# Performance work log

Measured on AMD Instinct MI355X. Metric: run time of the kernel, lower is better.

Reference implementation:

```python
import jax, jax.numpy as jnp
import numpy as np

B, N, IN_CH = 16, 2048, 128
H, C = 4, 64
HC = H * C
E = 524288
NT = B * N
FC0, FC1 = 1024, 512
OMIC = 128
OUT = 2
LN_EPS = 1e-5


def setup_inputs() -> dict:
    key = jax.random.key(0)
    ks = jax.random.split(key, 32)
    s = 0.02
    d = {}
    d['x'] = jax.random.normal(ks[0], (NT, IN_CH), jnp.float32)
    d['edge_index'] = jax.random.randint(ks[1], (2, E), 0, NT, dtype=jnp.int64)
    # GATConv 1: Linear(IN_CH, H*C, bias=False), att_src/att_dst [H,C], bias [H*C]
    d['w1'] = jax.random.normal(ks[2], (IN_CH, HC), jnp.float32) * s
    d['att_src1'] = jax.random.normal(ks[3], (H, C), jnp.float32) * s
    d['att_dst1'] = jax.random.normal(ks[4], (H, C), jnp.float32) * s
    d['bias1'] = jnp.zeros((HC,), jnp.float32)
    d['pool1_w'] = jax.random.normal(ks[5], (HC, 1), jnp.float32) * s
    d['pool1_b'] = jnp.zeros((1,), jnp.float32)
    # GATConv 2: in = H*C
    d['w2'] = jax.random.normal(ks[6], (HC, HC), jnp.float32) * s
    d['att_src2'] = jax.random.normal(ks[7], (H, C), jnp.float32) * s
    d['att_dst2'] = jax.random.normal(ks[8], (H, C), jnp.float32) * s
    d['bias2'] = jnp.zeros((HC,), jnp.float32)
    d['pool2_w'] = jax.random.normal(ks[9], (HC, 1), jnp.float32) * s
    d['pool2_b'] = jnp.zeros((1,), jnp.float32)
    # LayerNorm(num_nodes)
    d['ln_w'] = jnp.ones((N,), jnp.float32)
    d['ln_b'] = jnp.zeros((N,), jnp.float32)
    # FC encoder: Linear(3N, FC0)+ELU, Linear(FC0, FC1)+ELU, Linear(FC1, OMIC)+ELU
    d['enc0_w'] = jax.random.normal(ks[10], (3 * N, FC0), jnp.float32) * s
    d['enc0_b'] = jnp.zeros((FC0,), jnp.float32)
    d['enc1_w'] = jax.random.normal(ks[11], (FC0, FC1), jnp.float32) * s
    d['enc1_b'] = jnp.zeros((FC1,), jnp.float32)
    d['enc2_w'] = jax.random.normal(ks[12], (FC1, OMIC), jnp.float32) * s
    d['enc2_b'] = jnp.zeros((OMIC,), jnp.float32)
    d['last_w'] = jax.random.normal(ks[13], (OMIC, OUT), jnp.float32) * s
    d['last_b'] = jnp.zeros((OUT,), jnp.float32)
    return d


def layer_norm(v, w, b):
    mu = jnp.mean(v, axis=-1, keepdims=True)
    var = jnp.mean((v - mu) ** 2, axis=-1, keepdims=True)
    return (v - mu) * jax.lax.rsqrt(var + LN_EPS) * w + b


def gat_conv(x, src, dst, w, att_src, att_dst, bias):
    # x: [NT, F_in] -> transformed per head [NT, H, C]
    xw = (x @ w).reshape(NT, H, C)
    a_src = jnp.einsum('nhc,hc->nh', xw, att_src)  # [NT, H]
    a_dst = jnp.einsum('nhc,hc->nh', xw, att_dst)
    alpha = jax.nn.leaky_relu(a_src[src] + a_dst[dst], negative_slope=0.2)  # [E', H]
    amax = jax.ops.segment_max(alpha, dst, num_segments=NT)
    ea = jnp.exp(alpha - amax[dst])
    denom = jax.ops.segment_sum(ea, dst, num_segments=NT)
    coef = ea / (denom[dst] + 1e-16)
    msg = xw[src] * coef[:, :, None]  # [E', H, C]
    out = jax.ops.segment_sum(msg, dst, num_segments=NT)
    return out.reshape(NT, HC) + bias


def reference(x, edge_index, w1, att_src1, att_dst1, bias1, pool1_w, pool1_b,
              w2, att_src2, att_dst2, bias2, pool2_w, pool2_b,
              ln_w, ln_b, enc0_w, enc0_b, enc1_w, enc1_b, enc2_w, enc2_b,
              last_w, last_b):
    # add self-loops (GATConv default)
    loops = jnp.arange(NT, dtype=edge_index.dtype)
    src = jnp.concatenate([edge_index[0], loops])
    dst = jnp.concatenate([edge_index[1], loops])
    # layer1 feature: per-node mean, densified to [B, N]
    x0 = layer_norm(jnp.mean(x, axis=-1).reshape(B, N), ln_w, ln_b)
    # GAT layer 1 (dropout is identity in eval)
    h = jax.nn.elu(gat_conv(x, src, dst, w1, att_src1, att_dst1, bias1))
    x1 = layer_norm((h @ pool1_w + pool1_b)[:, 0].reshape(B, N), ln_w, ln_b)
    # GAT layer 2
    h = jax.nn.elu(gat_conv(h, src, dst, w2, att_src2, att_dst2, bias2))
    x2 = layer_norm((h @ pool2_w + pool2_b)[:, 0].reshape(B, N), ln_w, ln_b)
    feat = jnp.concatenate([x0, x1, x2], axis=1)  # [B, 3N]
    e = jax.nn.elu(feat @ enc0_w + enc0_b)
    e = jax.nn.elu(e @ enc1_w + enc1_b)
    e = jax.nn.elu(e @ enc2_w + enc2_b)
    return e @ last_w + last_b  # [B, OUT]
```

## Files before the change

### kernel.cpp

```cpp
#include <hip/hip_runtime.h>
#include <math.h>

#define NTN 32768
#define BB 16
#define NN 2048
#define IN_CH 128
#define HC 256
#define EREAL 524288
#define ETOT (EREAL + NTN)
#define FC0 1024
#define FC1 512
#define OMIC 128
#define OUTD 2
#define CAP 96

#define PREP_BLKS (NTN / 4)
#define DEG_BLKS (EREAL / 256)
#define CASTW_BLKS ((HC * IN_CH + HC * HC) / 256)
#define GEMM_YB (NTN / 128)
#define FILL_YB 512

typedef __attribute__((ext_vector_type(8))) short bf16x8;
typedef __attribute__((ext_vector_type(4))) float f32x4;
typedef __attribute__((ext_vector_type(2))) float f32x2;

static __device__ __forceinline__ float wave_sum(float v) {
    for (int o = 32; o; o >>= 1) v += __shfl_xor(v, o);
    return v;
}
static __device__ __forceinline__ unsigned short f2bf(float f) {
    unsigned u = __float_as_uint(f);
    unsigned r = (u + 0x7fff + ((u >> 16) & 1)) >> 16;
    return (unsigned short)r;
}
static __device__ __forceinline__ void wave_sync() {
    asm volatile("s_waitcnt lgkmcnt(0)" ::: "memory");
    __builtin_amdgcn_sched_barrier(0);
}
static __device__ __forceinline__ void pkfma(f32x2& acc, f32x2 ab, f32x2 e2) {
    asm("v_pk_fma_f32 %0, %1, %2, %0" : "+v"(acc) : "v"(ab), "v"(e2));
}
static __device__ __forceinline__ void fma8pk(uint4 v, f32x2 e2, f32x2* acc) {
    f32x2 p;
    p.x = __uint_as_float(v.x << 16); p.y = __uint_as_float(v.x & 0xffff0000u);
    pkfma(acc[0], p, e2);
    p.x = __uint_as_float(v.y << 16); p.y = __uint_as_float(v.y & 0xffff0000u);
    pkfma(acc[1], p, e2);
    p.x = __uint_as_float(v.z << 16); p.y = __uint_as_float(v.z & 0xffff0000u);
    pkfma(acc[2], p, e2);
    p.x = __uint_as_float(v.w << 16); p.y = __uint_as_float(v.w & 0xffff0000u);
    pkfma(acc[3], p, e2);
}
static __device__ __forceinline__ void dot2bf(float& acc, unsigned px, unsigned pe) {
    asm("v_dot2_f32_bf16 %0, %1, %2, %0" : "+v"(acc) : "v"(px), "v"(pe));
}
static __device__ __forceinline__ void dot8x2(uint4 a, uint4 b, unsigned pe, float* acc) {
    unsigned p;
    p = __builtin_amdgcn_perm(a.x, b.x, 0x01000504u); dot2bf(acc[0], p, pe);
    p = __builtin_amdgcn_perm(a.x, b.x, 0x03020706u); dot2bf(acc[1], p, pe);
    p = __builtin_amdgcn_perm(a.y, b.y, 0x01000504u); dot2bf(acc[2], p, pe);
    p = __builtin_amdgcn_perm(a.y, b.y, 0x03020706u); dot2bf(acc[3], p, pe);
    p = __builtin_amdgcn_perm(a.z, b.z, 0x01000504u); dot2bf(acc[4], p, pe);
    p = __builtin_amdgcn_perm(a.z, b.z, 0x03020706u); dot2bf(acc[5], p, pe);
    p = __builtin_amdgcn_perm(a.w, b.w, 0x01000504u); dot2bf(acc[6], p, pe);
    p = __builtin_amdgcn_perm(a.w, b.w, 0x03020706u); dot2bf(acc[7], p, pe);
}

__global__ __launch_bounds__(256) void k_pre(
    const float* __restrict__ x, unsigned short* __restrict__ xb, float* __restrict__ xmean,
    const int* __restrict__ ei, int* __restrict__ deg, int* __restrict__ epos,
    const float* __restrict__ w1, const float* __restrict__ w2,
    unsigned short* __restrict__ w1t, unsigned short* __restrict__ w2t) {
    int b = blockIdx.x, t = threadIdx.x;
    if (b < PREP_BLKS) {
        int wave = t >> 6, lane = t & 63;
        int n = b * 4 + wave;
        float2 v = *(const float2*)(x + (size_t)n * IN_CH + lane * 2);
        ushort2 o;
        o.x = f2bf(v.x); o.y = f2bf(v.y);
        *(ushort2*)(xb + (size_t)n * IN_CH + lane * 2) = o;
        float s = wave_sum(v.x + v.y);
        if (lane == 0) xmean[n] = s * (1.0f / 128.0f);
    } else if (b < PREP_BLKS + DEG_BLKS) {
        int e = (b - PREP_BLKS) * 256 + t;
        int d = ei[EREAL + e];
        epos[e] = atomicAdd(&deg[d], 1);
    } else {
        int idx = (b - PREP_BLKS - DEG_BLKS) * 256 + t;
        if (idx < HC * IN_CH) {
            int n = idx / IN_CH, k = idx % IN_CH;
            w1t[idx] = f2bf(w1[(size_t)k * HC + n]);
        } else {
            int j = idx - HC * IN_CH;
            int n = j / HC, k = j % HC;
            w2t[j] = f2bf(w2[(size_t)k * HC + n]);
        }
    }
}

__global__ __launch_bounds__(1024) void k_scan(const int* __restrict__ deg, int* __restrict__ rowptr,
                                               int* __restrict__ csr) {
    __shared__ int sd[1024];
    int t = threadIdx.x;
    int base = t * 32;
    int loc[32];
    int s = 0;
#pragma unroll
    for (int j = 0; j < 32; j++) { int d = deg[base + j] + 1; loc[j] = d; s += d; }
    sd[t] = s; __syncthreads();
    for (int o = 1; o < 1024; o <<= 1) {
        int v = (t >= o) ? sd[t - o] : 0;
        __syncthreads();
        sd[t] += v;
        __syncthreads();
    }
    int run = sd[t] - s;
#pragma unroll
    for (int j = 0; j < 32; j++) {
        rowptr[base + j] = run;
        csr[run] = base + j;
        run += loc[j];
    }
    if (t == 1023) rowptr[NTN] = run;
}

__global__ __launch_bounds__(256) void k_gemm_mfma(
    const unsigned short* __restrict__ A, const unsigned short* __restrict__ Bt, int K,
    const float* __restrict__ attS, const float* __restrict__ attD,
    unsigned short* __restrict__ Cout, float* __restrict__ aS, float* __restrict__ aD,
    const int* __restrict__ ei, const int* __restrict__ epos,
    const int* __restrict__ rowptr, int* __restrict__ csr) {
    __shared__ unsigned short As[128][72];
    __shared__ unsigned short Bs[64][72];
    const int t = threadIdx.x;
    const int bx = blockIdx.x, by = blockIdx.y;
    if (by >= GEMM_YB) {
        int e = (((by - GEMM_YB) * 4 + bx)) * 256 + t;
        int s = ei[e], d = ei[EREAL + e];
        csr[rowptr[d] + 1 + epos[e]] = s;
        return;
    }
    const int lane = t & 63, wave = t >> 6;
    const int quad = lane >> 4, l16 = lane & 15;
    const int arow = t >> 1, acol = (t & 1) * 32;
    const int brow = t >> 2, bcol = (t & 3) * 16;
    const unsigned short* Ag = A + (size_t)(by * 128 + arow) * K + acol;
    const unsigned short* Bg = Bt + (size_t)(bx * 64 + brow) * K + bcol;
    f32x4 acc[2][4] = {};
    for (int k0 = 0; k0 < K; k0 += 64) {
        uint4 a0 = *(const uint4*)(Ag + k0);
        uint4 a1 = *(const uint4*)(Ag + k0 + 8);
        uint4 a2 = *(const uint4*)(Ag + k0 + 16);
        uint4 a3 = *(const uint4*)(Ag + k0 + 24);
        uint4 b0 = *(const uint4*)(Bg + k0);
        uint4 b1 = *(const uint4*)(Bg + k0 + 8);
        __syncthreads();
        *(uint4*)&As[arow][acol +  0] = a0;
        *(uint4*)&As[arow][acol +  8] = a1;
        *(uint4*)&As[arow][acol + 16] = a2;
        *(uint4*)&As[arow][acol + 24] = a3;
        *(uint4*)&Bs[brow][bcol +  0] = b0;
        *(uint4*)&Bs[brow][bcol +  8] = b1;
        __syncthreads();
#pragma unroll
        for (int kc = 0; kc < 64; kc += 32) {
            bf16x8 af[2], bfr[4];
#pragma unroll
            for (int mt = 0; mt < 2; mt++)
                af[mt] = *(const bf16x8*)&As[wave * 32 + mt * 16 + l16][kc + quad * 8];
#pragma unroll
            for (int nt = 0; nt < 4; nt++)
                bfr[nt] = *(const bf16x8*)&Bs[nt * 16 + l16][kc + quad * 8];
#pragma unroll
            for (int mt = 0; mt < 2; mt++)
#pragma unroll
                for (int nt = 0; nt < 4; nt++)
                    acc[mt][nt] = __builtin_amdgcn_mfma_f32_16x16x32_bf16(af[mt], bfr[nt], acc[mt][nt], 0, 0, 0);
        }
    }
    float as_l[4], ad_l[4];
#pragma unroll
    for (int nt = 0; nt < 4; nt++) {
        int gcol = bx * 64 + nt * 16 + l16;
        as_l[nt] = attS[gcol];
        ad_l[nt] = attD[gcol];
    }
#pragma unroll
    for (int mt = 0; mt < 2; mt++) {
#pragma unroll
        for (int reg = 0; reg < 4; reg++) {
            int grow = by * 128 + wave * 32 + mt * 16 + quad * 4 + reg;
            float ps = 0.f, pd = 0.f;
#pragma unroll
            for (int nt = 0; nt < 4; nt++) {
                float v = acc[mt][nt][reg];
                Cout[(size_t)grow * HC + bx * 64 + nt * 16 + l16] = f2bf(v);
                ps += v * as_l[nt];
                pd += v * ad_l[nt];
            }
            for (int o = 8; o; o >>= 1) { ps += __shfl_xor(ps, o); pd += __shfl_xor(pd, o); }
            if (l16 == 0) { aS[grow * 4 + bx] = ps; aD[grow * 4 + bx] = pd; }
        }
    }
}

__global__ __launch_bounds__(256) void k_agg(
    const unsigned short* __restrict__ xw, const float* __restrict__ aS, const float* __restrict__ aD,
    const int* __restrict__ rowptr, const int* __restrict__ csr,
    const float* __restrict__ bias, const float* __restrict__ poolw, const float* __restrict__ poolb,
    unsigned short* __restrict__ hout, float* __restrict__ xpre) {
    __shared__ float ea_s[4][CAP][4];
    __shared__ int   ss[4][CAP];
    int t = threadIdx.x;
    int w = t >> 6, lane = t & 63;
    int n = blockIdx.x * 4 + w;
    int beg = rowptr[n], end = rowptr[n + 1];
    int deg = end - beg;
    float4 ad4 = *(const float4*)(aD + n * 4);
    float l0 = 0.f, l1 = 0.f, l2 = 0.f, l3 = 0.f;
    if (deg <= CAP) {
        for (int i = lane; i < deg; i += 64) {
            int s = csr[beg + i];
            ss[w][i] = s << 9;
            float4 as4 = *(const float4*)(aS + s * 4);
            float a0 = as4.x + ad4.x; a0 = a0 > 0.f ? a0 : 0.2f * a0;
            float a1 = as4.y + ad4.y; a1 = a1 > 0.f ? a1 : 0.2f * a1;
            float a2 = as4.z + ad4.z; a2 = a2 > 0.f ? a2 : 0.2f * a2;
            float a3 = as4.w + ad4.w; a3 = a3 > 0.f ? a3 : 0.2f * a3;
            float4 e4;
            e4.x = __expf(a0); e4.y = __expf(a1); e4.z = __expf(a2); e4.w = __expf(a3);
            *(float4*)&ea_s[w][i][0] = e4;
        }
        wave_sync();
    } else {
        for (int i = lane; i < deg; i += 64) {
            int s = csr[beg + i];
            float4 as4 = *(const float4*)(aS + s * 4);
            float a0 = as4.x + ad4.x; a0 = a0 > 0.f ? a0 : 0.2f * a0; l0 += __expf(a0);
            float a1 = as4.y + ad4.y; a1 = a1 > 0.f ? a1 : 0.2f * a1; l1 += __expf(a1);
            float a2 = as4.z + ad4.z; a2 = a2 > 0.f ? a2 : 0.2f * a2; l2 += __expf(a2);
            float a3 = as4.w + ad4.w; a3 = a3 > 0.f ? a3 : 0.2f * a3; l3 += __expf(a3);
        }
        l0 = wave_sum(l0); l1 = wave_sum(l1); l2 = wave_sum(l2); l3 = wave_sum(l3);
    }
    int l31 = lane & 31, hi = lane >> 5;
    int head = l31 >> 3;
    float acc8[8] = {};
    f32x2 accF[4] = {};
    unsigned tb = (unsigned)(l31 * 16);
    const char* xwb_ = (const char*)xw;
    if (deg <= CAP) {
        int i = 0;
        for (; i + 16 <= deg; i += 16) {
            int iA = i + 8 * hi;
            int o0 = ss[w][iA], o1 = ss[w][iA + 1], o2 = ss[w][iA + 2], o3 = ss[w][iA + 3];
            int o4 = ss[w][iA + 4], o5 = ss[w][iA + 5], o6 = ss[w][iA + 6], o7 = ss[w][iA + 7];
            float e0 = ea_s[w][iA][head],     e1 = ea_s[w][iA + 1][head];
            float e2 = ea_s[w][iA + 2][head], e3 = ea_s[w][iA + 3][head];
            float e4 = ea_s[w][iA + 4][head], e5 = ea_s[w][iA + 5][head];
            float e6 = ea_s[w][iA + 6][head], e7 = ea_s[w][iA + 7][head];
            uint4 v0 = *(const uint4*)(xwb_ + ((unsigned)o0 + tb));
            uint4 v1 = *(const uint4*)(xwb_ + ((unsigned)o1 + tb));
            uint4 v2 = *(const uint4*)(xwb_ + ((unsigned)o2 + tb));
            uint4 v3 = *(const uint4*)(xwb_ + ((unsigned)o3 + tb));
            uint4 v4 = *(const uint4*)(xwb_ + ((unsigned)o4 + tb));
            uint4 v5 = *(const uint4*)(xwb_ + ((unsigned)o5 + tb));
            uint4 v6 = *(const uint4*)(xwb_ + ((unsigned)o6 + tb));
            uint4 v7 = *(const uint4*)(xwb_ + ((unsigned)o7 + tb));
            unsigned p01, p23, p45, p67;
            asm("v_cvt_pk_bf16_f32 %0, %1, %2" : "=v"(p01) : "v"(e0), "v"(e1));
            asm("v_cvt_pk_bf16_f32 %0, %1, %2" : "=v"(p23) : "v"(e2), "v"(e3));
            asm("v_cvt_pk_bf16_f32 %0, %1, %2" : "=v"(p45) : "v"(e4), "v"(e5));
            asm("v_cvt_pk_bf16_f32 %0, %1, %2" : "=v"(p67) : "v"(e6), "v"(e7));
            dot8x2(v0, v1, p01, acc8);
            dot8x2(v2, v3, p23, acc8);
            dot8x2(v4, v5, p45, acc8);
            dot8x2(v6, v7, p67, acc8);
        }
        for (; i + 8 <= deg; i += 8) {
            int iA = i + 4 * hi;
            int o0 = ss[w][iA], o1 = ss[w][iA + 1], o2 = ss[w][iA + 2], o3 = ss[w][iA + 3];
            float e0 = ea_s[w][iA][head],     e1 = ea_s[w][iA + 1][head];
            float e2 = ea_s[w][iA + 2][head], e3 = ea_s[w][iA + 3][head];
            uint4 v0 = *(const uint4*)(xwb_ + ((unsigned)o0 + tb));
            uint4 v1 = *(const uint4*)(xwb_ + ((unsigned)o1 + tb));
            uint4 v2 = *(const uint4*)(xwb_ + ((unsigned)o2 + tb));
            uint4 v3 = *(const uint4*)(xwb_ + ((unsigned)o3 + tb));
            unsigned p01, p23;
            asm("v_cvt_pk_bf16_f32 %0, %1, %2" : "=v"(p01) : "v"(e0), "v"(e1));
            asm("v_cvt_pk_bf16_f32 %0, %1, %2" : "=v"(p23) : "v"(e2), "v"(e3));
            dot8x2(v0, v1, p01, acc8);
            dot8x2(v2, v3, p23, acc8);
        }
        for (; i + 4 <= deg; i += 4) {
            int iA = i + 2 * hi;
            int o0 = ss[w][iA], o1 = ss[w][iA + 1];
            float e0 = ea_s[w][iA][head], e1 = ea_s[w][iA + 1][head];
            unsigned pe;
            asm("v_cvt_pk_bf16_f32 %0, %1, %2" : "=v"(pe) : "v"(e0), "v"(e1));
            uint4 v0 = *(const uint4*)(xwb_ + ((unsigned)o0 + tb));
            uint4 v1 = *(const uint4*)(xwb_ + ((unsigned)o1 + tb));
            dot8x2(v0, v1, pe, acc8);
        }
        if (i < deg) {
            int iA = i + 2 * hi, iB = iA + 1;
            bool okA = iA < deg, okB = iB < deg;
            int ia = okA ? iA : 0;
            int ib = okB ? iB : 0;
            int o0 = ss[w][ia], o1 = ss[w][ib];
            float e0 = okA ? ea_s[w][ia][head] : 0.f;
            float e1 = okB ? ea_s[w][ib][head] : 0.f;
            unsigned pe;
            asm("v_cvt_pk_bf16_f32 %0, %1, %2" : "=v"(pe) : "v"(e0), "v"(e1));
            uint4 v0 = *(const uint4*)(xwb_ + ((unsigned)o0 + tb));
            uint4 v1 = *(const uint4*)(xwb_ + ((unsigned)o1 + tb));
            dot8x2(v0, v1, pe, acc8);
        }
    } else {
        const unsigned short* xwc = xw + l31 * 8;
        float adh = head == 0 ? ad4.x : head == 1 ? ad4.y : head == 2 ? ad4.z : ad4.w;
        for (int i = beg; i < end; i += 2) {
            int idx = i + hi;
            bool ok = idx < end;
            int sA = csr[ok ? idx : beg];
            float a = aS[sA * 4 + head] + adh;
            a = a > 0.f ? a : 0.2f * a;
            float eA = ok ? __expf(a) : 0.f;
            uint4 vA = *(const uint4*)(xwc + (size_t)sA * HC);
            f32x2 eA2; eA2.x = eA; eA2.y = eA;
            fma8pk(vA, eA2, accF);
        }
    }
    float r8[8];
#pragma unroll
    for (int j = 0; j < 8; j++) {
        float v = acc8[j] + accF[j >> 1][j & 1];
        v += __shfl_xor(v, 32);
        r8[j] = v;
    }
    if (hi == 0) {
        float ilh;
        if (deg <= CAP) {
            float lsum = 0.f;
            for (int j = (l31 & 7); j < deg; j += 8) lsum += ea_s[w][j][head];
            lsum += __shfl_xor(lsum, 1);
            lsum += __shfl_xor(lsum, 2);
            lsum += __shfl_xor(lsum, 4);
            ilh = 1.0f / (lsum + 1e-16f);
        } else {
            float lh = head == 0 ? l0 : head == 1 ? l1 : head == 2 ? l2 : l3;
            ilh = 1.0f / (lh + 1e-16f);
        }
        float4 b0 = *(const float4*)(bias + l31 * 8);
        float4 b1 = *(const float4*)(bias + l31 * 8 + 4);
        float r[8];
        r[0] = r8[0] * ilh + b0.x;
        r[1] = r8[1] * ilh + b0.y;
        r[2] = r8[2] * ilh + b0.z;
        r[3] = r8[3] * ilh + b0.w;
        r[4] = r8[4] * ilh + b1.x;
        r[5] = r8[5] * ilh + b1.y;
        r[6] = r8[6] * ilh + b1.z;
        r[7] = r8[7] * ilh + b1.w;
#pragma unroll
        for (int j = 0; j < 8; j++) r[j] = r[j] > 0.f ? r[j] : expm1f(r[j]);
        if (hout) {
            uint4 o;
            o.x = (unsigned)f2bf(r[0]) | ((unsigned)f2bf(r[1]) << 16);
            o.y = (unsigned)f2bf(r[2]) | ((unsigned)f2bf(r[3]) << 16);
            o.z = (unsigned)f2bf(r[4]) | ((unsigned)f2bf(r[5]) << 16);
            o.w = (unsigned)f2bf(r[6]) | ((unsigned)f2bf(r[7]) << 16);
            *(uint4*)(hout + (size_t)n * HC + l31 * 8) = o;
        }
        float4 w0 = *(const float4*)(poolw + l31 * 8);
        float4 w1v = *(const float4*)(poolw + l31 * 8 + 4);
        float p = r[0] * w0.x + r[1] * w0.y + r[2] * w0.z + r[3] * w0.w +
                  r[4] * w1v.x + r[5] * w1v.y + r[6] * w1v.z + r[7] * w1v.w;
        for (int o = 16; o; o >>= 1) p += __shfl_xor(p, o);
        if (l31 == 0) xpre[n] = p + poolb[0];
    }
}

__global__ __launch_bounds__(256) void k_ln3(const float* __restrict__ xmean, const float* __restrict__ x1pre,
                                             const float* __restrict__ x2pre, const float* __restrict__ lw,
                                             const float* __restrict__ lb, float* __restrict__ feat) {
    __shared__ float r0[256], r1[256];
    int b = blockIdx.x, t = threadIdx.x;
    int row = b & 15, seg = b >> 4;
    const float* src = (seg == 0 ? xmean : seg == 1 ? x1pre : x2pre) + (size_t)row * NN;
    float* dst = feat + (size_t)row * (3 * NN) + seg * NN;
    float v[8];
    float s = 0.f, s2 = 0.f;
#pragma unroll
    for (int j = 0; j < 8; j++) {
        float x = src[t + j * 256];
        v[j] = x; s += x; s2 += x * x;
    }
    r0[t] = s; r1[t] = s2; __syncthreads();
    for (int o = 128; o; o >>= 1) {
        if (t < o) { r0[t] += r0[t + o]; r1[t] += r1[t + o]; }
        __syncthreads();
    }
    float mu = r0[0] * (1.0f / NN);
    float var = r1[0] * (1.0f / NN) - mu * mu;
    float rs = rsqrtf(var + 1e-5f);
#pragma unroll
    for (int j = 0; j < 8; j++) {
        int idx = t + j * 256;
        dst[idx] = (v[j] - mu) * rs * lw[idx] + lb[idx];
    }
}

template<int KC>
__global__ __launch_bounds__(256) void k_fc_splitk(const float* __restrict__ In, const float* __restrict__ W,
                                                   float* __restrict__ partial, int K, int Nc) {
    __shared__ float in_s[16][KC];
    int t = threadIdx.x;
    int k0 = blockIdx.y * KC;
    for (int idx = t; idx < 16 * KC; idx += 256) {
        int r = idx / KC, kk = idx % KC;
        in_s[r][kk] = In[(size_t)r * K + k0 + kk];
    }
    __syncthreads();
    int col = blockIdx.x * 256 + t;
    if (col < Nc) {
        float acc[16] = {};
#pragma unroll
        for (int kk = 0; kk < KC; kk++) {
            float w = W[(size_t)(k0 + kk) * Nc + col];
#pragma unroll
            for (int r = 0; r < 16; r++) acc[r] += in_s[r][kk] * w;
        }
        float* pp = partial + ((size_t)blockIdx.y * 16) * Nc + col;
#pragma unroll
        for (int r = 0; r < 16; r++) pp[(size_t)r * Nc] = acc[r];
    }
}

template<int KS>
__global__ __launch_bounds__(256) void k_fc_reduce(const float* __restrict__ partial, const float* __restrict__ bias,
                                                   float* __restrict__ Out, int Nc) {
    __shared__ float sm[256];
    int t = threadIdx.x;
    int col = blockIdx.x * 32 + (t & 31);
    int r = blockIdx.y;
    int h = t >> 5;
    float s = 0.f;
#pragma unroll
    for (int i = 0; i < KS / 8; i++)
        s += partial[((size_t)(h + 8 * i) * 16 + r) * Nc + col];
    sm[t] = s;
    __syncthreads();
    if (t < 32) {
        float v = sm[t] + sm[t + 32] + sm[t + 64] + sm[t + 96] +
                  sm[t + 128] + sm[t + 160] + sm[t + 192] + sm[t + 224];
        v += bias[col];
        v = v > 0.f ? v : expm1f(v);
        Out[(size_t)r * Nc + col] = v;
    }
}

__global__ __launch_bounds__(256) void k_last(const float* __restrict__ In, const float* __restrict__ W,
                                              const float* __restrict__ b, float* __restrict__ Out) {
    int t = threadIdx.x;
    int r = t >> 4, c = (t >> 3) & 1, ksub = t & 7;
    float s = 0.f;
#pragma unroll
    for (int k = 0; k < OMIC / 8; k++) s += In[r * OMIC + k * 8 + ksub] * W[(k * 8 + ksub) * OUTD + c];
    for (int o = 1; o < 8; o <<= 1) s += __shfl_xor(s, o);
    if (ksub == 0) Out[r * OUTD + c] = s + b[c];
}

extern "C" void kernel_launch(void* const* d_in, const int* in_sizes, int n_in,
                              void* d_out, int out_size, void* d_ws, size_t ws_size,
                              hipStream_t stream) {
    (void)in_sizes; (void)n_in; (void)out_size; (void)ws_size;
    const float* x        = (const float*)d_in[0];
    const int*   ei       = (const int*)d_in[1];
    const float* w1       = (const float*)d_in[2];
    const float* att_src1 = (const float*)d_in[3];
    const float* att_dst1 = (const float*)d_in[4];
    const float* bias1    = (const float*)d_in[5];
    const float* pool1_w  = (const float*)d_in[6];
    const float* pool1_b  = (const float*)d_in[7];
    const float* w2       = (const float*)d_in[8];
    const float* att_src2 = (const float*)d_in[9];
    const float* att_dst2 = (const float*)d_in[10];
    const float* bias2    = (const float*)d_in[11];
    const float* pool2_w  = (const float*)d_in[12];
    const float* pool2_b  = (const float*)d_in[13];
    const float* ln_w     = (const float*)d_in[14];
    const float* ln_b     = (const float*)d_in[15];
    const float* enc0_w   = (const float*)d_in[16];
    const float* enc0_b   = (const float*)d_in[17];
    const float* enc1_w   = (const float*)d_in[18];
    const float* enc1_b   = (const float*)d_in[19];
    const float* enc2_w   = (const float*)d_in[20];
    const float* enc2_b   = (const float*)d_in[21];
    const float* last_w   = (const float*)d_in[22];
    const float* last_b   = (const float*)d_in[23];
    float* out = (float*)d_out;

    char* p = (char*)d_ws;
    auto alloc = [&](size_t bytes) -> void* {
        void* r = (void*)p;
        p += (bytes + 255) & ~(size_t)255;
        return r;
    };
    unsigned short* xwb  = (unsigned short*)alloc((size_t)NTN * HC * 2);
    unsigned short* hb   = (unsigned short*)alloc((size_t)NTN * HC * 2);
    unsigned short* xb   = (unsigned short*)alloc((size_t)NTN * IN_CH * 2);
    unsigned short* w1t  = (unsigned short*)alloc((size_t)HC * IN_CH * 2);
    unsigned short* w2t  = (unsigned short*)alloc((size_t)HC * HC * 2);
    float* a_src  = (float*)alloc((size_t)NTN * 4 * 4);
    float* a_dst  = (float*)alloc((size_t)NTN * 4 * 4);
    float* xmean  = (float*)alloc((size_t)NTN * 4);
    float* x1pre  = (float*)alloc((size_t)NTN * 4);
    float* x2pre  = (float*)alloc((size_t)NTN * 4);
    float* feat   = (float*)alloc((size_t)BB * 3 * NN * 4);
    float* e0     = (float*)alloc((size_t)BB * FC0 * 4);
    float* e1     = (float*)alloc((size_t)BB * FC1 * 4);
    float* e2     = (float*)alloc((size_t)BB * OMIC * 4);
    float* part0  = (float*)alloc((size_t)96 * 16 * FC0 * 4);
    float* part1  = (float*)alloc((size_t)64 * 16 * FC1 * 4);
    float* part2  = (float*)alloc((size_t)32 * 16 * OMIC * 4);
    int*   deg    = (int*)alloc((size_t)NTN * 4);
    int*   rowptr = (int*)alloc((size_t)(NTN + 1) * 4);
    int*   epos   = (int*)alloc((size_t)EREAL * 4);
    int*   csr    = (int*)alloc((size_t)ETOT * 4);

    hipMemsetAsync(deg, 0, (size_t)NTN * 4, stream);

    k_pre<<<PREP_BLKS + DEG_BLKS + CASTW_BLKS, 256, 0, stream>>>(
        x, xb, xmean, ei, deg, epos, w1, w2, w1t, w2t);
    k_scan<<<1, 1024, 0, stream>>>(deg, rowptr, csr);

    k_gemm_mfma<<<dim3(4, GEMM_YB + FILL_YB), 256, 0, stream>>>(
        xb, w1t, IN_CH, att_src1, att_dst1, xwb, a_src, a_dst, ei, epos, rowptr, csr);
    k_agg<<<NTN / 4, 256, 0, stream>>>(xwb, a_src, a_dst, rowptr, csr, bias1, pool1_w, pool1_b, hb, x1pre);

    k_gemm_mfma<<<dim3(4, GEMM_YB), 256, 0, stream>>>(
        hb, w2t, HC, att_src2, att_dst2, xwb, a_src, a_dst, ei, epos, rowptr, csr);
    k_agg<<<NTN / 4, 256, 0, stream>>>(xwb, a_src, a_dst, rowptr, csr, bias2, pool2_w, pool2_b, (unsigned short*)nullptr, x2pre);

    k_ln3<<<48, 256, 0, stream>>>(xmean, x1pre, x2pre, ln_w, ln_b, feat);

    k_fc_splitk<64><<<dim3(4, 96), 256, 0, stream>>>(feat, enc0_w, part0, 3 * NN, FC0);
    k_fc_reduce<96><<<dim3(FC0 / 32, 16), 256, 0, stream>>>(part0, enc0_b, e0, FC0);
    k_fc_splitk<16><<<dim3(2, 64), 256, 0, stream>>>(e0, enc1_w, part1, FC0, FC1);
    k_fc_reduce<64><<<dim3(FC1 / 32, 16), 256, 0, stream>>>(part1, enc1_b, e1, FC1);
    k_fc_splitk<16><<<dim3(1, 32), 256, 0, stream>>>(e1, enc2_w, part2, FC1, OMIC);
    k_fc_reduce<32><<<dim3(OMIC / 32, 16), 256, 0, stream>>>(part2, enc2_b, e2, OMIC);
    k_last<<<1, 256, 0, stream>>>(e2, last_w, last_b, out);
}
```

Before: 315.7 us.

## Fuse LayerNorm and FC encoder head into one cooperative kernel with grid syncs

Replaces the eight small launches (LayerNorm, three split-K FC layers with their reductions, and the final linear) with a single cooperative kernel of 384 blocks that separates the stages with grid-wide syncs. The aim is to remove per-launch overhead and inter-kernel gaps in the tail of the pipeline. In exchange it adds grid-barrier cost, leaves many blocks idle in the later stages, and makes the split-K inner loop non-templated, with a runtime KC and no unrolling.

Result: slower. 660.7 us (+109.3%).

```diff
diff --git a/kernel.cpp b/kernel.cpp
--- a/kernel.cpp
+++ b/kernel.cpp
@@ -1,5 +1,8 @@
 #include <hip/hip_runtime.h>
+#include <hip/hip_cooperative_groups.h>
 #include <math.h>
+
+namespace cg = cooperative_groups;
 
 #define NTN 32768
 #define BB 16
@@ -381,94 +384,108 @@
     }
 }
 
-__global__ __launch_bounds__(256) void k_ln3(const float* __restrict__ xmean, const float* __restrict__ x1pre,
-                                             const float* __restrict__ x2pre, const float* __restrict__ lw,
-                                             const float* __restrict__ lb, float* __restrict__ feat) {
-    __shared__ float r0[256], r1[256];
-    int b = blockIdx.x, t = threadIdx.x;
-    int row = b & 15, seg = b >> 4;
-    const float* src = (seg == 0 ? xmean : seg == 1 ? x1pre : x2pre) + (size_t)row * NN;
-    float* dst = feat + (size_t)row * (3 * NN) + seg * NN;
-    float v[8];
-    float s = 0.f, s2 = 0.f;
-#pragma unroll
-    for (int j = 0; j < 8; j++) {
-        float x = src[t + j * 256];
-        v[j] = x; s += x; s2 += x * x;
-    }
-    r0[t] = s; r1[t] = s2; __syncthreads();
-    for (int o = 128; o; o >>= 1) {
-        if (t < o) { r0[t] += r0[t + o]; r1[t] += r1[t + o]; }
-        __syncthreads();
-    }
-    float mu = r0[0] * (1.0f / NN);
-    float var = r1[0] * (1.0f / NN) - mu * mu;
-    float rs = rsqrtf(var + 1e-5f);
-#pragma unroll
-    for (int j = 0; j < 8; j++) {
-        int idx = t + j * 256;
-        dst[idx] = (v[j] - mu) * rs * lw[idx] + lb[idx];
-    }
-}
-
-template<int KC>
-__global__ __launch_bounds__(256) void k_fc_splitk(const float* __restrict__ In, const float* __restrict__ W,
-                                                   float* __restrict__ partial, int K, int Nc) {
-    __shared__ float in_s[16][KC];
-    int t = threadIdx.x;
-    int k0 = blockIdx.y * KC;
+
+static __device__ __forceinline__ void splitk_body(
+    const float* __restrict__ In, const float* __restrict__ W, float* __restrict__ partial,
+    int K, int Nc, int KC, int bx, int by, int t, float* in_s ) {
+    int k0 = by * KC;
     for (int idx = t; idx < 16 * KC; idx += 256) {
         int r = idx / KC, kk = idx % KC;
-        in_s[r][kk] = In[(size_t)r * K + k0 + kk];
+        in_s[r * KC + kk] = In[(size_t)r * K + k0 + kk];
     }
     __syncthreads();
-    int col = blockIdx.x * 256 + t;
+    int col = bx * 256 + t;
     if (col < Nc) {
         float acc[16] = {};
-#pragma unroll
         for (int kk = 0; kk < KC; kk++) {
             float w = W[(size_t)(k0 + kk) * Nc + col];
 #pragma unroll
-            for (int r = 0; r < 16; r++) acc[r] += in_s[r][kk] * w;
-        }
-        float* pp = partial + ((size_t)blockIdx.y * 16) * Nc + col;
+            for (int r = 0; r < 16; r++) acc[r] += in_s[r * KC + kk] * w;
+        }
+        float* pp = partial + ((size_t)by * 16) * Nc + col;
 #pragma unroll
         for (int r = 0; r < 16; r++) pp[(size_t)r * Nc] = acc[r];
     }
 }
 
 template<int KS>
-__global__ __launch_bounds__(256) void k_fc_reduce(const float* __restrict__ partial, const float* __restrict__ bias,
-                                                   float* __restrict__ Out, int Nc) {
-    __shared__ float sm[256];
-    int t = threadIdx.x;
-    int col = blockIdx.x * 32 + (t & 31);
-    int r = blockIdx.y;
-    int h = t >> 5;
-    float s = 0.f;
-#pragma unroll
-    for (int i = 0; i < KS / 8; i++)
-        s += partial[((size_t)(h + 8 * i) * 16 + r) * Nc + col];
-    sm[t] = s;
-    __syncthreads();
-    if (t < 32) {
-        float v = sm[t] + sm[t + 32] + sm[t + 64] + sm[t + 96] +
-                  sm[t + 128] + sm[t + 160] + sm[t + 192] + sm[t + 224];
-        v += bias[col];
-        v = v > 0.f ? v : expm1f(v);
-        Out[(size_t)r * Nc + col] = v;
-    }
-}
-
-__global__ __launch_bounds__(256) void k_last(const float* __restrict__ In, const float* __restrict__ W,
-                                              const float* __restrict__ b, float* __restrict__ Out) {
-    int t = threadIdx.x;
-    int r = t >> 4, c = (t >> 3) & 1, ksub = t & 7;
-    float s = 0.f;
-#pragma unroll
-    for (int k = 0; k < OMIC / 8; k++) s += In[r * OMIC + k * 8 + ksub] * W[(k * 8 + ksub) * OUTD + c];
-    for (int o = 1; o < 8; o <<= 1) s += __shfl_xor(s, o);
-    if (ksub == 0) Out[r * OUTD + c] = s + b[c];
+static __device__ __forceinline__ void reduce_body(
+    const float* __restrict__ partial, const float* __restrict__ bias, float* __restrict__ Out,
+    int Nc, int b, int t, int nb) {
+    for (int idx = b * 256 + t; idx < 16 * Nc; idx += nb * 256) {
+        int r = idx / Nc, col = idx - r * Nc;
+        float s = 0.f;
+#pragma unroll 8
+        for (int k = 0; k < KS; k++) s += partial[((size_t)k * 16 + r) * Nc + col];
+        s += bias[col];
+        Out[(size_t)r * Nc + col] = s > 0.f ? s : expm1f(s);
+    }
+}
+
+#define HEAD_BLKS 384
+
+__global__ __launch_bounds__(256) void k_head(
+    const float* __restrict__ xmean, const float* __restrict__ x1pre, const float* __restrict__ x2pre,
+    const float* __restrict__ lw, const float* __restrict__ lb, float* __restrict__ feat,
+    const float* __restrict__ enc0_w, const float* __restrict__ enc0_b,
+    const float* __restrict__ enc1_w, const float* __restrict__ enc1_b,
+    const float* __restrict__ enc2_w, const float* __restrict__ enc2_b,
+    const float* __restrict__ last_w, const float* __restrict__ last_b,
+    float* __restrict__ e0, float* __restrict__ e1, float* __restrict__ e2,
+    float* __restrict__ part0, float* __restrict__ part1, float* __restrict__ part2,
+    float* __restrict__ out) {
+    cg::grid_group gg = cg::this_grid();
+    __shared__ float lds[16 * 64];
+    int b = blockIdx.x, t = threadIdx.x;
+
+    if (b < 48) {
+        float* r0 = lds;
+        float* r1 = lds + 256;
+        int row = b & 15, seg = b >> 4;
+        const float* src = (seg == 0 ? xmean : seg == 1 ? x1pre : x2pre) + (size_t)row * NN;
+        float* dst = feat + (size_t)row * (3 * NN) + seg * NN;
+        float v[8];
+        float s = 0.f, s2 = 0.f;
+#pragma unroll
+        for (int j = 0; j < 8; j++) {
+            float x = src[t + j * 256];
+            v[j] = x; s += x; s2 += x * x;
+        }
+        r0[t] = s; r1[t] = s2; __syncthreads();
+        for (int o = 128; o; o >>= 1) {
+            if (t < o) { r0[t] += r0[t + o]; r1[t] += r1[t + o]; }
+            __syncthreads();
+        }
+        float mu = r0[0] * (1.0f / NN);
+        float var = r1[0] * (1.0f / NN) - mu * mu;
+        float rs = rsqrtf(var + 1e-5f);
+#pragma unroll
+        for (int j = 0; j < 8; j++) {
+            int idx = t + j * 256;
+            dst[idx] = (v[j] - mu) * rs * lw[idx] + lb[idx];
+        }
+    }
+    gg.sync();
+    splitk_body(feat, enc0_w, part0, 3 * NN, FC0, 64, b & 3, b >> 2, t, lds);
+    gg.sync();
+    reduce_body<96>(part0, enc0_b, e0, FC0, b, t, HEAD_BLKS);
+    gg.sync();
+    if (b < 128) splitk_body(e0, enc1_w, part1, FC0, FC1, 16, b & 1, b >> 1, t, lds);
+    gg.sync();
+    reduce_body<64>(part1, enc1_b, e1, FC1, b, t, HEAD_BLKS);
+    gg.sync();
+    if (b < 32) splitk_body(e1, enc2_w, part2, FC1, OMIC, 16, 0, b, t, lds);
+    gg.sync();
+    reduce_body<32>(part2, enc2_b, e2, OMIC, b, t, HEAD_BLKS);
+    gg.sync();
+    if (b == 0) {
+        int r = t >> 4, c = (t >> 3) & 1, ksub = t & 7;
+        float s = 0.f;
+#pragma unroll
+        for (int k = 0; k < OMIC / 8; k++) s += e2[r * OMIC + k * 8 + ksub] * last_w[(k * 8 + ksub) * OUTD + c];
+        for (int o = 1; o < 8; o <<= 1) s += __shfl_xor(s, o);
+        if (ksub == 0) out[r * OUTD + c] = s + last_b[c];
+    }
 }
 
 extern "C" void kernel_launch(void* const* d_in, const int* in_sizes, int n_in,
@@ -543,13 +560,15 @@
         hb, w2t, HC, att_src2, att_dst2, xwb, a_src, a_dst, ei, epos, rowptr, csr);
     k_agg<<<NTN / 4, 256, 0, stream>>>(xwb, a_src, a_dst, rowptr, csr, bias2, pool2_w, pool2_b, (unsigned short*)nullptr, x2pre);
 
-    k_ln3<<<48, 256, 0, stream>>>(xmean, x1pre, x2pre, ln_w, ln_b, feat);
-
-    k_fc_splitk<64><<<dim3(4, 96), 256, 0, stream>>>(feat, enc0_w, part0, 3 * NN, FC0);
-    k_fc_reduce<96><<<dim3(FC0 / 32, 16), 256, 0, stream>>>(part0, enc0_b, e0, FC0);
-    k_fc_splitk<16><<<dim3(2, 64), 256, 0, stream>>>(e0, enc1_w, part1, FC0, FC1);
-    k_fc_reduce<64><<<dim3(FC1 / 32, 16), 256, 0, stream>>>(part1, enc1_b, e1, FC1);
-    k_fc_splitk<16><<<dim3(1, 32), 256, 0, stream>>>(e1, enc2_w, part2, FC1, OMIC);
-    k_fc_reduce<32><<<dim3(OMIC / 32, 16), 256, 0, stream>>>(part2, enc2_b, e2, OMIC);
-    k_last<<<1, 256, 0, stream>>>(e2, last_w, last_b, out);
-}
+    {
+        unsigned short* hn = (unsigned short*)nullptr; (void)hn;
+        void* args[] = {
+            (void*)&xmean, (void*)&x1pre, (void*)&x2pre, (void*)&ln_w, (void*)&ln_b, (void*)&feat,
+            (void*)&enc0_w, (void*)&enc0_b, (void*)&enc1_w, (void*)&enc1_b,
+            (void*)&enc2_w, (void*)&enc2_b, (void*)&last_w, (void*)&last_b,
+            (void*)&e0, (void*)&e1, (void*)&e2,
+            (void*)&part0, (void*)&part1, (void*)&part2, (void*)&out
+        };
+        hipLaunchCooperativeKernel((const void*)k_head, dim3(HEAD_BLKS), dim3(256), args, 0, stream);
+    }
+}
```

## Fuse LayerNorm stats into producers and fold split-K reductions into next FC

Applied to the files above, without the earlier changes.

LayerNorm sum and sum-of-squares are now accumulated with per-block atomics inside k_pre and k_agg, so the separate k_ln3 kernel goes away and normalization is applied while k_fc0 loads its inputs. Each split-K reduce kernel is folded into the following FC layer (and into the final linear), which removes four launches and the intermediate buffers. The cost is float atomics, which make the statistics order-nondeterministic, a one-pass variance formula, and redundant partial-sum reads in every consumer block.

Result: slower. 782.6 us (+147.9%).

```diff
diff --git a/kernel.cpp b/kernel.cpp
--- a/kernel.cpp
+++ b/kernel.cpp
@@ -70,9 +70,11 @@
     const float* __restrict__ x, unsigned short* __restrict__ xb, float* __restrict__ xmean,
     const int* __restrict__ ei, int* __restrict__ deg, int* __restrict__ epos,
     const float* __restrict__ w1, const float* __restrict__ w2,
-    unsigned short* __restrict__ w1t, unsigned short* __restrict__ w2t) {
+    unsigned short* __restrict__ w1t, unsigned short* __restrict__ w2t,
+    float* __restrict__ stats0) {
     int b = blockIdx.x, t = threadIdx.x;
     if (b < PREP_BLKS) {
+        __shared__ float sb[4];
         int wave = t >> 6, lane = t & 63;
         int n = b * 4 + wave;
         float2 v = *(const float2*)(x + (size_t)n * IN_CH + lane * 2);
@@ -80,7 +82,16 @@
         o.x = f2bf(v.x); o.y = f2bf(v.y);
         *(ushort2*)(xb + (size_t)n * IN_CH + lane * 2) = o;
         float s = wave_sum(v.x + v.y);
-        if (lane == 0) xmean[n] = s * (1.0f / 128.0f);
+        if (lane == 0) { float m = s * (1.0f / 128.0f); xmean[n] = m; sb[wave] = m; }
+        __syncthreads();
+        if (t == 0) {
+            float su = 0.f, sq = 0.f;
+#pragma unroll
+            for (int j = 0; j < 4; j++) { float m = sb[j]; su += m; sq += m * m; }
+            int row = b >> 9;
+            atomicAdd(&stats0[row * 2], su);
+            atomicAdd(&stats0[row * 2 + 1], sq);
+        }
     } else if (b < PREP_BLKS + DEG_BLKS) {
         int e = (b - PREP_BLKS) * 256 + t;
         int d = ei[EREAL + e];
@@ -208,9 +219,10 @@
     const unsigned short* __restrict__ xw, const float* __restrict__ aS, const float* __restrict__ aD,
     const int* __restrict__ rowptr, const int* __restrict__ csr,
     const float* __restrict__ bias, const float* __restrict__ poolw, const float* __restrict__ poolb,
-    unsigned short* __restrict__ hout, float* __restrict__ xpre) {
+    unsigned short* __restrict__ hout, float* __restrict__ xpre, float* __restrict__ stats) {
     __shared__ float ea_s[4][CAP][4];
     __shared__ int   ss[4][CAP];
+    __shared__ float pshare[4];
     int t = threadIdx.x;
     int w = t >> 6, lane = t & 63;
     int n = blockIdx.x * 4 + w;
@@ -377,98 +389,143 @@
         float p = r[0] * w0.x + r[1] * w0.y + r[2] * w0.z + r[3] * w0.w +
                   r[4] * w1v.x + r[5] * w1v.y + r[6] * w1v.z + r[7] * w1v.w;
         for (int o = 16; o; o >>= 1) p += __shfl_xor(p, o);
-        if (l31 == 0) xpre[n] = p + poolb[0];
-    }
-}
-
-__global__ __launch_bounds__(256) void k_ln3(const float* __restrict__ xmean, const float* __restrict__ x1pre,
-                                             const float* __restrict__ x2pre, const float* __restrict__ lw,
-                                             const float* __restrict__ lb, float* __restrict__ feat) {
-    __shared__ float r0[256], r1[256];
-    int b = blockIdx.x, t = threadIdx.x;
-    int row = b & 15, seg = b >> 4;
-    const float* src = (seg == 0 ? xmean : seg == 1 ? x1pre : x2pre) + (size_t)row * NN;
-    float* dst = feat + (size_t)row * (3 * NN) + seg * NN;
-    float v[8];
-    float s = 0.f, s2 = 0.f;
-#pragma unroll
-    for (int j = 0; j < 8; j++) {
-        float x = src[t + j * 256];
-        v[j] = x; s += x; s2 += x * x;
-    }
-    r0[t] = s; r1[t] = s2; __syncthreads();
-    for (int o = 128; o; o >>= 1) {
-        if (t < o) { r0[t] += r0[t + o]; r1[t] += r1[t + o]; }
-        __syncthreads();
-    }
-    float mu = r0[0] * (1.0f / NN);
-    float var = r1[0] * (1.0f / NN) - mu * mu;
-    float rs = rsqrtf(var + 1e-5f);
-#pragma unroll
-    for (int j = 0; j < 8; j++) {
+        if (l31 == 0) { float v = p + poolb[0]; xpre[n] = v; pshare[w] = v; }
+    }
+    __syncthreads();
+    if (t == 0) {
+        float su = 0.f, sq = 0.f;
+#pragma unroll
+        for (int j = 0; j < 4; j++) { float v = pshare[j]; su += v; sq += v * v; }
+        int row = blockIdx.x >> 9;
+        atomicAdd(&stats[row * 2], su);
+        atomicAdd(&stats[row * 2 + 1], sq);
+    }
+}
+
+
+__global__ __launch_bounds__(256) void k_fc0(
+    const float* __restrict__ xmean, const float* __restrict__ x1pre, const float* __restrict__ x2pre,
+    const float* __restrict__ stats0, const float* __restrict__ stats1, const float* __restrict__ stats2,
+    const float* __restrict__ lw, const float* __restrict__ lb,
+    const float* __restrict__ W, float* __restrict__ partial) {
+    __shared__ float in_s[16][64];
+    __shared__ float murs[16][2];
+    int t = threadIdx.x;
+    int bx = blockIdx.x, by = blockIdx.y;
+    int k0 = by * 64;
+    int seg = k0 >> 11;
+    int c0 = k0 & (NN - 1);
+    const float* src = seg == 0 ? xmean : seg == 1 ? x1pre : x2pre;
+    const float* st  = seg == 0 ? stats0 : seg == 1 ? stats1 : stats2;
+    if (t < 16) {
+        float su = st[t * 2], sq = st[t * 2 + 1];
+        float mu = su * (1.0f / NN);
+        float var = sq * (1.0f / NN) - mu * mu;
+        murs[t][0] = mu;
+        murs[t][1] = rsqrtf(var + 1e-5f);
+    }
+    __syncthreads();
+#pragma unroll
+    for (int j = 0; j < 4; j++) {
         int idx = t + j * 256;
-        dst[idx] = (v[j] - mu) * rs * lw[idx] + lb[idx];
-    }
-}
-
-template<int KC>
-__global__ __launch_bounds__(256) void k_fc_splitk(const float* __restrict__ In, const float* __restrict__ W,
-                                                   float* __restrict__ partial, int K, int Nc) {
-    __shared__ float in_s[16][KC];
+        int r = idx >> 6, kk = idx & 63;
+        int c = c0 + kk;
+        float xv = src[(size_t)r * NN + c];
+        in_s[r][kk] = (xv - murs[r][0]) * murs[r][1] * lw[c] + lb[c];
+    }
+    __syncthreads();
+    int col = bx * 256 + t;
+    float acc[16] = {};
+    for (int kk = 0; kk < 64; kk++) {
+        float wv = W[(size_t)(k0 + kk) * FC0 + col];
+#pragma unroll
+        for (int r = 0; r < 16; r++) acc[r] += in_s[r][kk] * wv;
+    }
+    float* pp = partial + ((size_t)by * 16) * FC0 + col;
+#pragma unroll
+    for (int r = 0; r < 16; r++) pp[(size_t)r * FC0] = acc[r];
+}
+
+__global__ __launch_bounds__(256) void k_fc1(
+    const float* __restrict__ part0, const float* __restrict__ b0,
+    const float* __restrict__ W, float* __restrict__ partial) {
+    __shared__ float in_s[16][16];
     int t = threadIdx.x;
-    int k0 = blockIdx.y * KC;
-    for (int idx = t; idx < 16 * KC; idx += 256) {
-        int r = idx / KC, kk = idx % KC;
-        in_s[r][kk] = In[(size_t)r * K + k0 + kk];
+    int bx = blockIdx.x, by = blockIdx.y;
+    int k0 = by * 16;
+    {
+        int r = t >> 4, kk = t & 15;
+        float s = 0.f;
+#pragma unroll 8
+        for (int k = 0; k < 96; k++) s += part0[((size_t)(k * 16) + r) * FC0 + (k0 + kk)];
+        s += b0[k0 + kk];
+        in_s[r][kk] = s > 0.f ? s : expm1f(s);
     }
     __syncthreads();
-    int col = blockIdx.x * 256 + t;
-    if (col < Nc) {
+    int col = bx * 256 + t;
+    float acc[16] = {};
+#pragma unroll
+    for (int kk = 0; kk < 16; kk++) {
+        float wv = W[(size_t)(k0 + kk) * FC1 + col];
+#pragma unroll
+        for (int r = 0; r < 16; r++) acc[r] += in_s[r][kk] * wv;
+    }
+    float* pp = partial + ((size_t)by * 16) * FC1 + col;
+#pragma unroll
+    for (int r = 0; r < 16; r++) pp[(size_t)r * FC1] = acc[r];
+}
+
+__global__ __launch_bounds__(256) void k_fc2(
+    const float* __restrict__ part1, const float* __restrict__ b1,
+    const float* __restrict__ W, float* __restrict__ partial) {
+    __shared__ float in_s[16][16];
+    int t = threadIdx.x;
+    int by = blockIdx.x;
+    int k0 = by * 16;
+    {
+        int r = t >> 4, kk = t & 15;
+        float s = 0.f;
+#pragma unroll 8
+        for (int k = 0; k < 64; k++) s += part1[((size_t)(k * 16) + r) * FC1 + (k0 + kk)];
+        s += b1[k0 + kk];
+        in_s[r][kk] = s > 0.f ? s : expm1f(s);
+    }
+    __syncthreads();
+    if (t < OMIC) {
+        int col = t;
         float acc[16] = {};
 #pragma unroll
-        for (int kk = 0; kk < KC; kk++) {
-            float w = W[(size_t)(k0 + kk) * Nc + col];
-#pragma unroll
-            for (int r = 0; r < 16; r++) acc[r] += in_s[r][kk] * w;
-        }
-        float* pp = partial + ((size_t)blockIdx.y * 16) * Nc + col;
-#pragma unroll
-        for (int r = 0; r < 16; r++) pp[(size_t)r * Nc] = acc[r];
-    }
-}
-
-template<int KS>
-__global__ __launch_bounds__(256) void k_fc_reduce(const float* __restrict__ partial, const float* __restrict__ bias,
-                                                   float* __restrict__ Out, int Nc) {
-    __shared__ float sm[256];
+        for (int kk = 0; kk < 16; kk++) {
+            float wv = W[(size_t)(k0 + kk) * OMIC + col];
+#pragma unroll
+            for (int r = 0; r < 16; r++) acc[r] += in_s[r][kk] * wv;
+        }
+        float* pp = partial + ((size_t)by * 16) * OMIC + col;
+#pragma unroll
+        for (int r = 0; r < 16; r++) pp[(size_t)r * OMIC] = acc[r];
+    }
+}
+
+__global__ __launch_bounds__(256) void k_last2(
+    const float* __restrict__ part2, const float* __restrict__ b2,
+    const float* __restrict__ W, const float* __restrict__ bl, float* __restrict__ Out) {
+    __shared__ float e2s[16][OMIC];
     int t = threadIdx.x;
-    int col = blockIdx.x * 32 + (t & 31);
-    int r = blockIdx.y;
-    int h = t >> 5;
-    float s = 0.f;
-#pragma unroll
-    for (int i = 0; i < KS / 8; i++)
-        s += partial[((size_t)(h + 8 * i) * 16 + r) * Nc + col];
-    sm[t] = s;
+    for (int idx = t; idx < 16 * OMIC; idx += 256) {
+        int r = idx >> 7, c = idx & 127;
+        float s = 0.f;
+#pragma unroll 8
+        for (int k = 0; k < 32; k++) s += part2[((size_t)(k * 16) + r) * OMIC + c];
+        s += b2[c];
+        e2s[r][c] = s > 0.f ? s : expm1f(s);
+    }
     __syncthreads();
-    if (t < 32) {
-        float v = sm[t] + sm[t + 32] + sm[t + 64] + sm[t + 96] +
-                  sm[t + 128] + sm[t + 160] + sm[t + 192] + sm[t + 224];
-        v += bias[col];
-        v = v > 0.f ? v : expm1f(v);
-        Out[(size_t)r * Nc + col] = v;
-    }
-}
-
-__global__ __launch_bounds__(256) void k_last(const float* __restrict__ In, const float* __restrict__ W,
-                                              const float* __restrict__ b, float* __restrict__ Out) {
-    int t = threadIdx.x;
     int r = t >> 4, c = (t >> 3) & 1, ksub = t & 7;
     float s = 0.f;
 #pragma unroll
-    for (int k = 0; k < OMIC / 8; k++) s += In[r * OMIC + k * 8 + ksub] * W[(k * 8 + ksub) * OUTD + c];
+    for (int k = 0; k < OMIC / 8; k++) s += e2s[r][k * 8 + ksub] * W[(k * 8 + ksub) * OUTD + c];
     for (int o = 1; o < 8; o <<= 1) s += __shfl_xor(s, o);
-    if (ksub == 0) Out[r * OUTD + c] = s + b[c];
+    if (ksub == 0) Out[r * OUTD + c] = s + bl[c];
 }
 
 extern "C" void kernel_launch(void* const* d_in, const int* in_sizes, int n_in,
@@ -517,39 +574,34 @@
     float* xmean  = (float*)alloc((size_t)NTN * 4);
     float* x1pre  = (float*)alloc((size_t)NTN * 4);
     float* x2pre  = (float*)alloc((size_t)NTN * 4);
-    float* feat   = (float*)alloc((size_t)BB * 3 * NN * 4);
-    float* e0     = (float*)alloc((size_t)BB * FC0 * 4);
-    float* e1     = (float*)alloc((size_t)BB * FC1 * 4);
-    float* e2     = (float*)alloc((size_t)BB * OMIC * 4);
     float* part0  = (float*)alloc((size_t)96 * 16 * FC0 * 4);
     float* part1  = (float*)alloc((size_t)64 * 16 * FC1 * 4);
     float* part2  = (float*)alloc((size_t)32 * 16 * OMIC * 4);
-    int*   deg    = (int*)alloc((size_t)NTN * 4);
+    int*   deg    = (int*)alloc((size_t)NTN * 4 + 384);
+    float* stats0 = (float*)(deg + NTN);
+    float* stats1 = stats0 + 32;
+    float* stats2 = stats0 + 64;
     int*   rowptr = (int*)alloc((size_t)(NTN + 1) * 4);
     int*   epos   = (int*)alloc((size_t)EREAL * 4);
     int*   csr    = (int*)alloc((size_t)ETOT * 4);
 
-    hipMemsetAsync(deg, 0, (size_t)NTN * 4, stream);
+    hipMemsetAsync(deg, 0, (size_t)NTN * 4 + 384, stream);
 
     k_pre<<<PREP_BLKS + DEG_BLKS + CASTW_BLKS, 256, 0, stream>>>(
-        x, xb, xmean, ei, deg, epos, w1, w2, w1t, w2t);
+        x, xb, xmean, ei, deg, epos, w1, w2, w1t, w2t, stats0);
     k_scan<<<1, 1024, 0, stream>>>(deg, rowptr, csr);
 
     k_gemm_mfma<<<dim3(4, GEMM_YB + FILL_YB), 256, 0, stream>>>(
         xb, w1t, IN_CH, att_src1, att_dst1, xwb, a_src, a_dst, ei, epos, rowptr, csr);
-    k_agg<<<NTN / 4, 256, 0, stream>>>(xwb, a_src, a_dst, rowptr, csr, bias1, pool1_w, pool1_b, hb, x1pre);
+    k_agg<<<NTN / 4, 256, 0, stream>>>(xwb, a_src, a_dst, rowptr, csr, bias1, pool1_w, pool1_b, hb, x1pre, stats1);
 
     k_gemm_mfma<<<dim3(4, GEMM_YB), 256, 0, stream>>>(
         hb, w2t, HC, att_src2, att_dst2, xwb, a_src, a_dst, ei, epos, rowptr, csr);
-    k_agg<<<NTN / 4, 256, 0, stream>>>(xwb, a_src, a_dst, rowptr, csr, bias2, pool2_w, pool2_b, (unsigned short*)nullptr, x2pre);
-
-    k_ln3<<<48, 256, 0, stream>>>(xmean, x1pre, x2pre, ln_w, ln_b, feat);
-
-    k_fc_splitk<64><<<dim3(4, 96), 256, 0, stream>>>(feat, enc0_w, part0, 3 * NN, FC0);
-    k_fc_reduce<96><<<dim3(FC0 / 32, 16), 256, 0, stream>>>(part0, enc0_b, e0, FC0);
-    k_fc_splitk<16><<<dim3(2, 64), 256, 0, stream>>>(e0, enc1_w, part1, FC0, FC1);
-    k_fc_reduce<64><<<dim3(FC1 / 32, 16), 256, 0, stream>>>(part1, enc1_b, e1, FC1);
-    k_fc_splitk<16><<<dim3(1, 32), 256, 0, stream>>>(e1, enc2_w, part2, FC1, OMIC);
-    k_fc_reduce<32><<<dim3(OMIC / 32, 16), 256, 0, stream>>>(part2, enc2_b, e2, OMIC);
-    k_last<<<1, 256, 0, stream>>>(e2, last_w, last_b, out);
-}
+    k_agg<<<NTN / 4, 256, 0, stream>>>(xwb, a_src, a_dst, rowptr, csr, bias2, pool2_w, pool2_b, (unsigned short*)nullptr, x2pre, stats2);
+
+    k_fc0<<<dim3(4, 96), 256, 0, stream>>>(xmean, x1pre, x2pre, stats0, stats1, stats2,
+                                           ln_w, ln_b, enc0_w, part0);
+    k_fc1<<<dim3(2, 64), 256, 0, stream>>>(part0, enc0_b, enc1_w, part1);
+    k_fc2<<<32, 256, 0, stream>>>(part1, enc1_b, enc2_w, part2);
+    k_last2<<<1, 256, 0, stream>>>(part2, enc2_b, last_w, last_b, out);
+}
```
